# Optimization experiments

Hardware: AMD Instinct MI355X
Metric: run time of the kernel (lower is better)

## Reference

```python
import jax, jax.numpy as jnp
import numpy as np

N, E = 50000, 800000
IN, HID, OUT, T = 96, 128, 64, 8
THETA = 0.5


def setup_inputs() -> dict:
    key = jax.random.key(0)
    ks = jax.random.split(key, 8)
    x = jax.random.normal(ks[0], (N, IN), dtype=jnp.float32)
    edge_weight = jax.random.uniform(ks[1], (E,), dtype=jnp.float32)
    W1 = jax.random.normal(ks[2], (IN, HID), dtype=jnp.float32) * (2.0 / np.sqrt(IN + HID))
    W2 = jax.random.normal(ks[3], (HID, OUT), dtype=jnp.float32) * (2.0 / np.sqrt(HID + OUT))
    # Bernoulli(1 - theta) masks, fixed per MC sample (created in __init__)
    mask1 = (jax.random.uniform(ks[4], (T, IN, HID)) < (1.0 - THETA)).astype(jnp.float32)
    mask2 = (jax.random.uniform(ks[5], (T, HID, OUT)) < (1.0 - THETA)).astype(jnp.float32)
    src = jax.random.randint(ks[6], (E,), 0, N, dtype=jnp.int32)
    dst = jax.random.randint(ks[7], (E,), 0, N, dtype=jnp.int32)
    return {"x": x, "edge_weight": edge_weight, "W1": W1, "W2": W2,
            "mask1": mask1, "mask2": mask2, "src": src, "dst": dst}


def _spmm(feat, edge_weight, src, dst, n_nodes):
    # u_mul_e('feat','edge_weight') followed by fn.sum onto dst nodes
    msg = feat[src] * edge_weight[:, None]          # [E, D]
    return jax.ops.segment_sum(msg, dst, num_segments=n_nodes)  # [N, D]


def reference(x, edge_weight, W1, W2, mask1, mask2, src, dst):
    n = x.shape[0]
    # first aggregation is mask-independent -> compute once, share across T samples
    agg1 = _spmm(x, edge_weight, src, dst, n)       # [N, IN]

    def per_sample(m1, m2):
        h = jax.nn.relu(agg1 @ (W1 * m1))           # [N, HID]
        agg2 = _spmm(h, edge_weight, src, dst, n)   # [N, HID]
        return agg2 @ (W2 * m2)                     # [N, OUT]

    # stack of the T per-sample outputs (torch version returns a list)
    return jax.vmap(per_sample)(mask1, mask2)       # [T, N, OUT]
```

## Files before the change

### kernel.cpp

```cpp
#include <hip/hip_runtime.h>

#define N_NODES 50000
#define N_EDGES 800000
#define IN_F 96
#define HID_F 128
#define OUT_F 64
#define T_S 8
#define SCAN_B 196

typedef __attribute__((ext_vector_type(8))) short short8;
typedef __attribute__((ext_vector_type(4))) float float4v;
typedef __attribute__((ext_vector_type(2))) unsigned uint2v;
typedef __attribute__((ext_vector_type(4))) unsigned uint4v;

__device__ __forceinline__ float bf2f(unsigned short h) {
    unsigned u = ((unsigned)h) << 16;
    float f;
    __builtin_memcpy(&f, &u, 4);
    return f;
}
__device__ __forceinline__ unsigned short f2bf(float f) {
    unsigned u;
    __builtin_memcpy(&u, &f, 4);
    unsigned r = (u + 0x7fffu + ((u >> 16) & 1u)) >> 16;
    return (unsigned short)r;
}
__device__ __forceinline__ float bf_lo(unsigned u) {
    unsigned v = u << 16;
    float f;
    __builtin_memcpy(&f, &v, 4);
    return f;
}
__device__ __forceinline__ float bf_hi(unsigned u) {
    unsigned v = u & 0xffff0000u;
    float f;
    __builtin_memcpy(&f, &v, 4);
    return f;
}

__global__ void k_count(const int* __restrict__ dst, int* __restrict__ cnt) {
    int e = blockIdx.x * 256 + threadIdx.x;
    if (e < N_EDGES) atomicAdd(&cnt[dst[e]], 1);
}

__global__ __launch_bounds__(256) void k_scan1(const int* __restrict__ cnt,
                                               int* __restrict__ excl,
                                               int* __restrict__ blockSums) {
    __shared__ int buf[256];
    int tid = threadIdx.x;
    int idx = blockIdx.x * 256 + tid;
    int v = (idx < N_NODES) ? cnt[idx] : 0;
    buf[tid] = v;
    __syncthreads();
    for (int off = 1; off < 256; off <<= 1) {
        int t = buf[tid];
        int u = (tid >= off) ? buf[tid - off] : 0;
        __syncthreads();
        buf[tid] = t + u;
        __syncthreads();
    }
    int incl = buf[tid];
    if (idx < N_NODES) excl[idx] = incl - v;
    if (tid == 255) blockSums[blockIdx.x] = incl;
}

__global__ __launch_bounds__(256) void k_scan2(const int* __restrict__ blockSums,
                                               int* __restrict__ blockOff) {
    __shared__ int buf[256];
    int tid = threadIdx.x;
    int v = (tid < SCAN_B) ? blockSums[tid] : 0;
    buf[tid] = v;
    __syncthreads();
    for (int off = 1; off < 256; off <<= 1) {
        int t = buf[tid];
        int u = (tid >= off) ? buf[tid - off] : 0;
        __syncthreads();
        buf[tid] = t + u;
        __syncthreads();
    }
    if (tid < SCAN_B) blockOff[tid] = buf[tid] - v;
}

__global__ __launch_bounds__(256) void k_scan3(const int* __restrict__ excl,
                                               const int* __restrict__ blockOff,
                                               int* __restrict__ row_ptr,
                                               int* __restrict__ cursor) {
    int idx = blockIdx.x * 256 + threadIdx.x;
    if (idx < N_NODES) {
        int p = excl[idx] + blockOff[blockIdx.x];
        row_ptr[idx] = p;
        cursor[idx] = p;
    }
    if (idx == 0) row_ptr[N_NODES] = N_EDGES;
}

__global__ void k_fill(const int* __restrict__ src, const int* __restrict__ dst,
                       const float* __restrict__ ew, int* __restrict__ cursor,
                       uint2v* __restrict__ csr) {
    int e = blockIdx.x * 256 + threadIdx.x;
    if (e < N_EDGES) {
        int d = dst[e];
        int pos = atomicAdd(&cursor[d], 1);
        uint2v c;
        c.x = (unsigned)src[e];
        c.y = __float_as_uint(ew[e]);
        __builtin_nontemporal_store(c, &csr[pos]);
    }
}

__global__ void k_xb(const float* __restrict__ x, unsigned short* __restrict__ xb) {
    int i = blockIdx.x * 256 + threadIdx.x;
    int idx = i * 4;
    if (idx < N_NODES * IN_F) {
        float4v v = __builtin_nontemporal_load((const float4v*)(x + idx));
        uint2v r;
        r.x = (unsigned)f2bf(v.x) | ((unsigned)f2bf(v.y) << 16);
        r.y = (unsigned)f2bf(v.z) | ((unsigned)f2bf(v.w) << 16);
        *(uint2v*)(xb + idx) = r;
    }
}

__global__ __launch_bounds__(256) void k_spmm1(const unsigned short* __restrict__ xb,
                                               const int* __restrict__ row_ptr,
                                               const uint2v* __restrict__ csr,
                                               unsigned short* __restrict__ agg1) {
    int wave = threadIdx.x >> 6, lane = threadIdx.x & 63;
    int node = blockIdx.x * 4 + wave;
    if (lane >= 48) return;
    int beg = row_ptr[node], end = row_ptr[node + 1];
    const unsigned* xrow = (const unsigned*)xb;
    float a0 = 0.f, a1 = 0.f;
    int e = beg;
    for (; e + 7 < end; e += 8) {
        uint2v c[8];
        unsigned d[8];
#pragma unroll
        for (int i = 0; i < 8; i++) c[i] = __builtin_nontemporal_load(&csr[e + i]);
#pragma unroll
        for (int i = 0; i < 8; i++) d[i] = xrow[(size_t)c[i].x * 48 + lane];
#pragma unroll
        for (int i = 0; i < 8; i++) {
            float wv = __uint_as_float(c[i].y);
            a0 = fmaf(wv, bf_lo(d[i]), a0);
            a1 = fmaf(wv, bf_hi(d[i]), a1);
        }
    }
    for (; e + 3 < end; e += 4) {
        uint2v c[4];
        unsigned d[4];
#pragma unroll
        for (int i = 0; i < 4; i++) c[i] = __builtin_nontemporal_load(&csr[e + i]);
#pragma unroll
        for (int i = 0; i < 4; i++) d[i] = xrow[(size_t)c[i].x * 48 + lane];
#pragma unroll
        for (int i = 0; i < 4; i++) {
            float wv = __uint_as_float(c[i].y);
            a0 = fmaf(wv, bf_lo(d[i]), a0);
            a1 = fmaf(wv, bf_hi(d[i]), a1);
        }
    }
    for (; e < end; e++) {
        uint2v c = __builtin_nontemporal_load(&csr[e]);
        float wv = __uint_as_float(c.y);
        unsigned d = xrow[(size_t)c.x * 48 + lane];
        a0 = fmaf(wv, bf_lo(d), a0);
        a1 = fmaf(wv, bf_hi(d), a1);
    }
    unsigned pk = (unsigned)f2bf(a0) | ((unsigned)f2bf(a1) << 16);
    __builtin_nontemporal_store(pk, (unsigned*)agg1 + (size_t)node * 48 + lane);
}

__global__ void k_wprep(const float* __restrict__ W1, const float* __restrict__ W2,
                        const float* __restrict__ m1, const float* __restrict__ m2,
                        unsigned short* __restrict__ wf) {
    int gid = blockIdx.x * 256 + threadIdx.x;
    if (gid >= T_S * 20480) return;
    int t = gid / 20480;
    int idx = gid % 20480;
    float val;
    if (idx < 12288) {
        int j = idx & 7, lane = (idx >> 3) & 63, fr = idx >> 9;
        int kk = fr >> 3, nt = fr & 7;
        int k = kk * 32 + (lane >> 4) * 8 + j;
        int n = nt * 16 + (lane & 15);
        val = W1[k * HID_F + n] * m1[((size_t)t * IN_F + k) * HID_F + n];
    } else {
        int i2 = idx - 12288;
        int j = i2 & 7, lane = (i2 >> 3) & 63, fr = i2 >> 9;
        int kk = fr >> 2, ot = fr & 3;
        int k = kk * 32 + (lane >> 4) * 8 + j;
        int o = ot * 16 + (lane & 15);
        val = W2[k * OUT_F + o] * m2[((size_t)t * HID_F + k) * OUT_F + o];
    }
    wf[gid] = f2bf(val);
}

__global__ __launch_bounds__(256) void k_gemm(const unsigned short* __restrict__ agg1,
                                              const unsigned short* __restrict__ wfrags,
                                              unsigned short* __restrict__ P, int tBase,
                                              int nodeStride, int tMul) {
    __shared__ __align__(16) unsigned short ldsW[20480];
    __shared__ __align__(16) unsigned short ldsH[4][2176];
    int t = tBase + blockIdx.y;
    const uint4* wsrc = (const uint4*)(wfrags + (size_t)t * 20480);
    uint4* wdst = (uint4*)ldsW;
    for (int i = threadIdx.x; i < 2560; i += 256) wdst[i] = wsrc[i];
    __syncthreads();

    int wave = threadIdx.x >> 6, lane = threadIdx.x & 63;
    int quad = lane >> 4, l15 = lane & 15;

    for (int it = 0; it < 4; it++) {
        int node = blockIdx.x * 256 + it * 64 + wave * 16 + l15;
        bool v = node < N_NODES;

        short8 a[3];
        if (v) {
            const unsigned short* ap = agg1 + (size_t)node * IN_F;
            a[0] = *(const short8*)(ap + 0 * 32 + quad * 8);
            a[1] = *(const short8*)(ap + 1 * 32 + quad * 8);
            a[2] = *(const short8*)(ap + 2 * 32 + quad * 8);
        } else {
            short8 z = {0, 0, 0, 0, 0, 0, 0, 0};
            a[0] = z; a[1] = z; a[2] = z;
        }

        for (int nt = 0; nt < 8; nt++) {
            float4v acc = {0.f, 0.f, 0.f, 0.f};
            for (int kk = 0; kk < 3; kk++) {
                short8 w = *(const short8*)&ldsW[(kk * 8 + nt) * 512 + lane * 8];
                acc = __builtin_amdgcn_mfma_f32_16x16x32_bf16(w, a[kk], acc, 0, 0, 0);
            }
            unsigned h0 = f2bf(fmaxf(acc[0], 0.f));
            unsigned h1 = f2bf(fmaxf(acc[1], 0.f));
            unsigned h2 = f2bf(fmaxf(acc[2], 0.f));
            unsigned h3 = f2bf(fmaxf(acc[3], 0.f));
            uint2 pk;
            pk.x = h0 | (h1 << 16);
            pk.y = h2 | (h3 << 16);
            *(uint2*)&ldsH[wave][l15 * 136 + nt * 16 + quad * 4] = pk;
        }

        short8 hf[4];
        for (int kk = 0; kk < 4; kk++)
            hf[kk] = *(const short8*)&ldsH[wave][l15 * 136 + kk * 32 + quad * 8];

        unsigned short* Pt = P + (size_t)node * nodeStride + (size_t)t * tMul;
        for (int ot = 0; ot < 4; ot++) {
            float4v acc = {0.f, 0.f, 0.f, 0.f};
            for (int kk = 0; kk < 4; kk++) {
                short8 w = *(const short8*)&ldsW[12288 + (kk * 4 + ot) * 512 + lane * 8];
                acc = __builtin_amdgcn_mfma_f32_16x16x32_bf16(w, hf[kk], acc, 0, 0, 0);
            }
            if (v) {
                uint2v pk;
                pk.x = (unsigned)f2bf(acc[0]) | ((unsigned)f2bf(acc[1]) << 16);
                pk.y = (unsigned)f2bf(acc[2]) | ((unsigned)f2bf(acc[3]) << 16);
                __builtin_nontemporal_store(pk, (uint2v*)(Pt + ot * 16 + quad * 4));
            }
        }
    }
}

__global__ __launch_bounds__(256) void k_spmm2(const unsigned short* __restrict__ P,
                                               const int* __restrict__ row_ptr,
                                               const uint2v* __restrict__ csr,
                                               float* __restrict__ out) {
    int wave = threadIdx.x >> 6, lane = threadIdx.x & 63;
    int node = blockIdx.x * 4 + wave;
    int beg = row_ptr[node], end = row_ptr[node + 1];
    const uint4v* Pl = (const uint4v*)P + lane;
    float acc[8] = {0.f, 0.f, 0.f, 0.f, 0.f, 0.f, 0.f, 0.f};
    int e = beg;
    for (; e + 7 < end; e += 8) {
        uint2v c[8];
        uint4v d[8];
#pragma unroll
        for (int i = 0; i < 8; i++) c[i] = __builtin_nontemporal_load(&csr[e + i]);
#pragma unroll
        for (int i = 0; i < 8; i++) d[i] = Pl[(size_t)c[i].x * 64];
#pragma unroll
        for (int i = 0; i < 8; i++) {
            float wv = __uint_as_float(c[i].y);
            acc[0] = fmaf(wv, bf_lo(d[i].x), acc[0]);
            acc[1] = fmaf(wv, bf_hi(d[i].x), acc[1]);
            acc[2] = fmaf(wv, bf_lo(d[i].y), acc[2]);
            acc[3] = fmaf(wv, bf_hi(d[i].y), acc[3]);
            acc[4] = fmaf(wv, bf_lo(d[i].z), acc[4]);
            acc[5] = fmaf(wv, bf_hi(d[i].z), acc[5]);
            acc[6] = fmaf(wv, bf_lo(d[i].w), acc[6]);
            acc[7] = fmaf(wv, bf_hi(d[i].w), acc[7]);
        }
    }
    for (; e + 3 < end; e += 4) {
        uint2v c[4];
        uint4v d[4];
#pragma unroll
        for (int i = 0; i < 4; i++) c[i] = __builtin_nontemporal_load(&csr[e + i]);
#pragma unroll
        for (int i = 0; i < 4; i++) d[i] = Pl[(size_t)c[i].x * 64];
#pragma unroll
        for (int i = 0; i < 4; i++) {
            float wv = __uint_as_float(c[i].y);
            acc[0] = fmaf(wv, bf_lo(d[i].x), acc[0]);
            acc[1] = fmaf(wv, bf_hi(d[i].x), acc[1]);
            acc[2] = fmaf(wv, bf_lo(d[i].y), acc[2]);
            acc[3] = fmaf(wv, bf_hi(d[i].y), acc[3]);
            acc[4] = fmaf(wv, bf_lo(d[i].z), acc[4]);
            acc[5] = fmaf(wv, bf_hi(d[i].z), acc[5]);
            acc[6] = fmaf(wv, bf_lo(d[i].w), acc[6]);
            acc[7] = fmaf(wv, bf_hi(d[i].w), acc[7]);
        }
    }
    for (; e < end; e++) {
        uint2v c = __builtin_nontemporal_load(&csr[e]);
        float wv = __uint_as_float(c.y);
        uint4v d = Pl[(size_t)c.x * 64];
        acc[0] = fmaf(wv, bf_lo(d.x), acc[0]);
        acc[1] = fmaf(wv, bf_hi(d.x), acc[1]);
        acc[2] = fmaf(wv, bf_lo(d.y), acc[2]);
        acc[3] = fmaf(wv, bf_hi(d.y), acc[3]);
        acc[4] = fmaf(wv, bf_lo(d.z), acc[4]);
        acc[5] = fmaf(wv, bf_hi(d.z), acc[5]);
        acc[6] = fmaf(wv, bf_lo(d.w), acc[6]);
        acc[7] = fmaf(wv, bf_hi(d.w), acc[7]);
    }
    int t = lane >> 3, o = (lane & 7) * 8;
    float* op = out + ((size_t)t * N_NODES + node) * OUT_F + o;
    float4v v0 = {acc[0], acc[1], acc[2], acc[3]};
    float4v v1 = {acc[4], acc[5], acc[6], acc[7]};
    __builtin_nontemporal_store(v0, (float4v*)op);
    __builtin_nontemporal_store(v1, (float4v*)(op + 4));
}

__global__ __launch_bounds__(512) void k_spmm2_1t(const unsigned short* __restrict__ P,
                                                  const int* __restrict__ row_ptr,
                                                  const uint2v* __restrict__ csr,
                                                  float* __restrict__ out) {
    int node = blockIdx.x * 8 + (threadIdx.x >> 6);
    int o = threadIdx.x & 63;
    if (node >= N_NODES) return;
    int beg = row_ptr[node], end = row_ptr[node + 1];
    const unsigned short* Pt = P + o;
    float a0 = 0.f, a1 = 0.f, a2 = 0.f, a3 = 0.f;
    int e = beg;
    for (; e + 3 < end; e += 4) {
        uint2v c0 = __builtin_nontemporal_load(&csr[e]);
        uint2v c1 = __builtin_nontemporal_load(&csr[e + 1]);
        uint2v c2 = __builtin_nontemporal_load(&csr[e + 2]);
        uint2v c3 = __builtin_nontemporal_load(&csr[e + 3]);
        a0 += __uint_as_float(c0.y) * bf2f(Pt[(size_t)c0.x * OUT_F]);
        a1 += __uint_as_float(c1.y) * bf2f(Pt[(size_t)c1.x * OUT_F]);
        a2 += __uint_as_float(c2.y) * bf2f(Pt[(size_t)c2.x * OUT_F]);
        a3 += __uint_as_float(c3.y) * bf2f(Pt[(size_t)c3.x * OUT_F]);
    }
    for (; e < end; e++) {
        uint2v c = __builtin_nontemporal_load(&csr[e]);
        a0 += __uint_as_float(c.y) * bf2f(Pt[(size_t)c.x * OUT_F]);
    }
    out[(size_t)node * OUT_F + o] = a0 + a1 + a2 + a3;
}

extern "C" void kernel_launch(void* const* d_in, const int* in_sizes, int n_in,
                              void* d_out, int out_size, void* d_ws, size_t ws_size,
                              hipStream_t stream) {
    const float* x = (const float*)d_in[0];
    const float* ew = (const float*)d_in[1];
    const float* W1 = (const float*)d_in[2];
    const float* W2 = (const float*)d_in[3];
    const float* m1 = (const float*)d_in[4];
    const float* m2 = (const float*)d_in[5];
    const int* src = (const int*)d_in[6];
    const int* dst = (const int*)d_in[7];
    float* out = (float*)d_out;

    char* w = (char*)d_ws;
    size_t off = 0;
    auto alloc = [&](size_t bytes) -> void* {
        void* p = (void*)(w + off);
        off += (bytes + 255) & ~(size_t)255;
        return p;
    };
    int* cnt = (int*)alloc((size_t)N_NODES * 4);
    int* row_ptr = (int*)alloc((size_t)(N_NODES + 1) * 4);
    int* cursor = (int*)alloc((size_t)N_NODES * 4);
    int* excl = (int*)alloc((size_t)N_NODES * 4);
    int* blockSums = (int*)alloc((size_t)SCAN_B * 4);
    int* blockOff = (int*)alloc((size_t)SCAN_B * 4);
    uint2v* csr = (uint2v*)alloc((size_t)N_EDGES * 8);
    unsigned short* agg1 = (unsigned short*)alloc((size_t)N_NODES * IN_F * 2);
    unsigned short* wf = (unsigned short*)alloc((size_t)T_S * 20480 * 2);

    size_t unionBase = off;
    size_t pBytesBatched = (size_t)T_S * N_NODES * OUT_F * 2;
    size_t xbBytes = (size_t)N_NODES * IN_F * 2;
    bool batched = ws_size >= unionBase + (pBytesBatched > xbBytes ? pBytesBatched : xbBytes);
    unsigned short* xb = (unsigned short*)(w + unionBase);
    unsigned short* P = (unsigned short*)(w + unionBase);
    if (!batched) {
        xb = (unsigned short*)(w + unionBase);
        P = (unsigned short*)(w + unionBase + ((xbBytes + 255) & ~(size_t)255));
    }

    hipMemsetAsync(cnt, 0, (size_t)N_NODES * 4, stream);
    k_count<<<N_EDGES / 256, 256, 0, stream>>>(dst, cnt);
    k_scan1<<<SCAN_B, 256, 0, stream>>>(cnt, excl, blockSums);
    k_scan2<<<1, 256, 0, stream>>>(blockSums, blockOff);
    k_scan3<<<SCAN_B, 256, 0, stream>>>(excl, blockOff, row_ptr, cursor);
    k_fill<<<N_EDGES / 256, 256, 0, stream>>>(src, dst, ew, cursor, csr);
    k_xb<<<(N_NODES * IN_F / 4 + 255) / 256, 256, 0, stream>>>(x, xb);
    k_spmm1<<<N_NODES / 4, 256, 0, stream>>>(xb, row_ptr, csr, agg1);
    k_wprep<<<(T_S * 20480) / 256, 256, 0, stream>>>(W1, W2, m1, m2, wf);

    if (batched) {
        k_gemm<<<dim3(196, 8), 256, 0, stream>>>(agg1, wf, P, 0, T_S * OUT_F, OUT_F);
        k_spmm2<<<N_NODES / 4, 256, 0, stream>>>(P, row_ptr, csr, out);
    } else {
        for (int t = 0; t < T_S; t++) {
            k_gemm<<<dim3(196, 1), 256, 0, stream>>>(agg1, wf, P, t, OUT_F, 0);
            k_spmm2_1t<<<6250, 512, 0, stream>>>(P, row_ptr, csr,
                                                 out + (size_t)t * N_NODES * OUT_F);
        }
    }
}
```

Baseline: 423.9 us.

## Split second SpMM into two half-sample passes and drop nontemporal hints

The batched second aggregation is split into two launches, each gathering 4 of the 8 samples (8 bytes per lane instead of 16). The goal is to halve the working set of the gathered P rows per pass so more of it stays in cache. Nontemporal load/store hints on CSR, agg1 and output are also replaced with ordinary accesses so those lines can be cached. The cost is reading the CSR and row pointers twice and making twice as many gather requests.

```diff
diff --git a/kernel.cpp b/kernel.cpp
--- a/kernel.cpp
+++ b/kernel.cpp
@@ -135,7 +135,7 @@
         uint2v c[8];
         unsigned d[8];
 #pragma unroll
-        for (int i = 0; i < 8; i++) c[i] = __builtin_nontemporal_load(&csr[e + i]);
+        for (int i = 0; i < 8; i++) c[i] = csr[e + i];
 #pragma unroll
         for (int i = 0; i < 8; i++) d[i] = xrow[(size_t)c[i].x * 48 + lane];
 #pragma unroll
@@ -149,7 +149,7 @@
         uint2v c[4];
         unsigned d[4];
 #pragma unroll
-        for (int i = 0; i < 4; i++) c[i] = __builtin_nontemporal_load(&csr[e + i]);
+        for (int i = 0; i < 4; i++) c[i] = csr[e + i];
 #pragma unroll
         for (int i = 0; i < 4; i++) d[i] = xrow[(size_t)c[i].x * 48 + lane];
 #pragma unroll
@@ -160,14 +160,14 @@
         }
     }
     for (; e < end; e++) {
-        uint2v c = __builtin_nontemporal_load(&csr[e]);
+        uint2v c = csr[e];
         float wv = __uint_as_float(c.y);
         unsigned d = xrow[(size_t)c.x * 48 + lane];
         a0 = fmaf(wv, bf_lo(d), a0);
         a1 = fmaf(wv, bf_hi(d), a1);
     }
-    unsigned pk = (unsigned)f2bf(a0) | ((unsigned)f2bf(a1) << 16);
-    __builtin_nontemporal_store(pk, (unsigned*)agg1 + (size_t)node * 48 + lane);
+    ((unsigned*)agg1)[(size_t)node * 48 + lane] =
+        (unsigned)f2bf(a0) | ((unsigned)f2bf(a1) << 16);
 }
 
 __global__ void k_wprep(const float* __restrict__ W1, const float* __restrict__ W2,
@@ -262,23 +262,23 @@
     }
 }
 
-__global__ __launch_bounds__(256) void k_spmm2(const unsigned short* __restrict__ P,
-                                               const int* __restrict__ row_ptr,
-                                               const uint2v* __restrict__ csr,
-                                               float* __restrict__ out) {
+__global__ __launch_bounds__(256) void k_spmm2h(const unsigned short* __restrict__ P,
+                                                const int* __restrict__ row_ptr,
+                                                const uint2v* __restrict__ csr,
+                                                float* __restrict__ out, int g) {
     int wave = threadIdx.x >> 6, lane = threadIdx.x & 63;
     int node = blockIdx.x * 4 + wave;
     int beg = row_ptr[node], end = row_ptr[node + 1];
-    const uint4v* Pl = (const uint4v*)P + lane;
-    float acc[8] = {0.f, 0.f, 0.f, 0.f, 0.f, 0.f, 0.f, 0.f};
+    const uint2v* Pl = (const uint2v*)P + g * 64 + lane;
+    float acc[4] = {0.f, 0.f, 0.f, 0.f};
     int e = beg;
     for (; e + 7 < end; e += 8) {
         uint2v c[8];
-        uint4v d[8];
-#pragma unroll
-        for (int i = 0; i < 8; i++) c[i] = __builtin_nontemporal_load(&csr[e + i]);
-#pragma unroll
-        for (int i = 0; i < 8; i++) d[i] = Pl[(size_t)c[i].x * 64];
+        uint2v d[8];
+#pragma unroll
+        for (int i = 0; i < 8; i++) c[i] = csr[e + i];
+#pragma unroll
+        for (int i = 0; i < 8; i++) d[i] = Pl[(size_t)c[i].x * 128];
 #pragma unroll
         for (int i = 0; i < 8; i++) {
             float wv = __uint_as_float(c[i].y);
@@ -286,19 +286,15 @@
             acc[1] = fmaf(wv, bf_hi(d[i].x), acc[1]);
             acc[2] = fmaf(wv, bf_lo(d[i].y), acc[2]);
             acc[3] = fmaf(wv, bf_hi(d[i].y), acc[3]);
-            acc[4] = fmaf(wv, bf_lo(d[i].z), acc[4]);
-            acc[5] = fmaf(wv, bf_hi(d[i].z), acc[5]);
-            acc[6] = fmaf(wv, bf_lo(d[i].w), acc[6]);
-            acc[7] = fmaf(wv, bf_hi(d[i].w), acc[7]);
         }
     }
     for (; e + 3 < end; e += 4) {
         uint2v c[4];
-        uint4v d[4];
-#pragma unroll
-        for (int i = 0; i < 4; i++) c[i] = __builtin_nontemporal_load(&csr[e + i]);
-#pragma unroll
-        for (int i = 0; i < 4; i++) d[i] = Pl[(size_t)c[i].x * 64];
+        uint2v d[4];
+#pragma unroll
+        for (int i = 0; i < 4; i++) c[i] = csr[e + i];
+#pragma unroll
+        for (int i = 0; i < 4; i++) d[i] = Pl[(size_t)c[i].x * 128];
 #pragma unroll
         for (int i = 0; i < 4; i++) {
             float wv = __uint_as_float(c[i].y);
@@ -306,31 +302,21 @@
             acc[1] = fmaf(wv, bf_hi(d[i].x), acc[1]);
             acc[2] = fmaf(wv, bf_lo(d[i].y), acc[2]);
             acc[3] = fmaf(wv, bf_hi(d[i].y), acc[3]);
-            acc[4] = fmaf(wv, bf_lo(d[i].z), acc[4]);
-            acc[5] = fmaf(wv, bf_hi(d[i].z), acc[5]);
-            acc[6] = fmaf(wv, bf_lo(d[i].w), acc[6]);
-            acc[7] = fmaf(wv, bf_hi(d[i].w), acc[7]);
         }
     }
     for (; e < end; e++) {
-        uint2v c = __builtin_nontemporal_load(&csr[e]);
+        uint2v c = csr[e];
         float wv = __uint_as_float(c.y);
-        uint4v d = Pl[(size_t)c.x * 64];
+        uint2v d = Pl[(size_t)c.x * 128];
         acc[0] = fmaf(wv, bf_lo(d.x), acc[0]);
         acc[1] = fmaf(wv, bf_hi(d.x), acc[1]);
         acc[2] = fmaf(wv, bf_lo(d.y), acc[2]);
         acc[3] = fmaf(wv, bf_hi(d.y), acc[3]);
-        acc[4] = fmaf(wv, bf_lo(d.z), acc[4]);
-        acc[5] = fmaf(wv, bf_hi(d.z), acc[5]);
-        acc[6] = fmaf(wv, bf_lo(d.w), acc[6]);
-        acc[7] = fmaf(wv, bf_hi(d.w), acc[7]);
-    }
-    int t = lane >> 3, o = (lane & 7) * 8;
+    }
+    int t = g * 4 + (lane >> 4), o = (lane & 15) * 4;
     float* op = out + ((size_t)t * N_NODES + node) * OUT_F + o;
     float4v v0 = {acc[0], acc[1], acc[2], acc[3]};
-    float4v v1 = {acc[4], acc[5], acc[6], acc[7]};
-    __builtin_nontemporal_store(v0, (float4v*)op);
-    __builtin_nontemporal_store(v1, (float4v*)(op + 4));
+    *(float4v*)op = v0;
 }
 
 __global__ __launch_bounds__(512) void k_spmm2_1t(const unsigned short* __restrict__ P,
@@ -345,17 +331,17 @@
     float a0 = 0.f, a1 = 0.f, a2 = 0.f, a3 = 0.f;
     int e = beg;
     for (; e + 3 < end; e += 4) {
-        uint2v c0 = __builtin_nontemporal_load(&csr[e]);
-        uint2v c1 = __builtin_nontemporal_load(&csr[e + 1]);
-        uint2v c2 = __builtin_nontemporal_load(&csr[e + 2]);
-        uint2v c3 = __builtin_nontemporal_load(&csr[e + 3]);
+        uint2v c0 = csr[e];
+        uint2v c1 = csr[e + 1];
+        uint2v c2 = csr[e + 2];
+        uint2v c3 = csr[e + 3];
         a0 += __uint_as_float(c0.y) * bf2f(Pt[(size_t)c0.x * OUT_F]);
         a1 += __uint_as_float(c1.y) * bf2f(Pt[(size_t)c1.x * OUT_F]);
         a2 += __uint_as_float(c2.y) * bf2f(Pt[(size_t)c2.x * OUT_F]);
         a3 += __uint_as_float(c3.y) * bf2f(Pt[(size_t)c3.x * OUT_F]);
     }
     for (; e < end; e++) {
-        uint2v c = __builtin_nontemporal_load(&csr[e]);
+        uint2v c = csr[e];
         a0 += __uint_as_float(c.y) * bf2f(Pt[(size_t)c.x * OUT_F]);
     }
     out[(size_t)node * OUT_F + o] = a0 + a1 + a2 + a3;
@@ -414,7 +400,8 @@
 
     if (batched) {
         k_gemm<<<dim3(196, 8), 256, 0, stream>>>(agg1, wf, P, 0, T_S * OUT_F, OUT_F);
-        k_spmm2<<<N_NODES / 4, 256, 0, stream>>>(P, row_ptr, csr, out);
+        k_spmm2h<<<N_NODES / 4, 256, 0, stream>>>(P, row_ptr, csr, out, 0);
+        k_spmm2h<<<N_NODES / 4, 256, 0, stream>>>(P, row_ptr, csr, out, 1);
     } else {
         for (int t = 0; t < T_S; t++) {
             k_gemm<<<dim3(196, 1), 256, 0, stream>>>(agg1, wf, P, t, OUT_F, 0);
```

Measured after the change: 418.7 us. About the same (-1.2%).
